# Kernel tuning notes

Hardware: AMD Instinct MI355X
Metric: run time of the kernel (lower is better)

Reference implementation:

```python
import jax, jax.numpy as jnp
import numpy as np

NUM_HEADS = 16
DIM_MODEL = 1024
DIM_K = DIM_MODEL // NUM_HEADS
B, S = 2, 2048


def _linear_params(key, d_in, d_out):
    kw, kb = jax.random.split(key)
    bound = 1.0 / np.sqrt(d_in)
    W = jax.random.uniform(kw, (d_out, d_in), jnp.float32, -bound, bound)
    b = jax.random.uniform(kb, (d_out,), jnp.float32, -bound, bound)
    return W, b


def setup_inputs() -> dict:
    key = jax.random.key(0)
    ks = jax.random.split(key, 7)
    Q_in = jax.random.normal(ks[0], (B, S, DIM_MODEL), jnp.float32)
    K_in = jax.random.normal(ks[1], (B, S, DIM_MODEL), jnp.float32)
    V_in = jax.random.normal(ks[2], (B, S, DIM_MODEL), jnp.float32)
    Wq, bq = _linear_params(ks[3], DIM_MODEL, DIM_MODEL)
    Wk, bk = _linear_params(ks[4], DIM_MODEL, DIM_MODEL)
    Wv, bv = _linear_params(ks[5], DIM_MODEL, DIM_MODEL)
    Wo, bo = _linear_params(ks[6], DIM_MODEL, DIM_MODEL)
    return {"Q_in": Q_in, "K_in": K_in, "V_in": V_in,
            "Wq": Wq, "bq": bq, "Wk": Wk, "bk": bk,
            "Wv": Wv, "bv": bv, "Wo": Wo, "bo": bo}


def reference(Q_in, K_in, V_in, Wq, bq, Wk, bk, Wv, bv, Wo, bo):
    # QKV projections (nn.Linear: x @ W.T + b)
    Q = Q_in @ Wq.T + bq
    K = K_in @ Wk.T + bk
    V = V_in @ Wv.T + bv
    # [B, S, D] -> [B, H, S, dk]
    def split_heads(x):
        return x.reshape(B, S, NUM_HEADS, DIM_K).transpose(0, 2, 1, 3)
    Qh, Kh, Vh = split_heads(Q), split_heads(K), split_heads(V)
    # Scaled dot-product attention
    scale = 1.0 / np.sqrt(DIM_K)
    scores = jnp.einsum('bhqd,bhkd->bhqk', Qh, Kh) * scale  # [B,H,S,S]
    attn = jax.nn.softmax(scores, axis=-1)
    out = jnp.einsum('bhqk,bhkd->bhqd', attn, Vh)  # [B,H,S,dk]
    # Merge heads -> [B, S, D]
    out = out.transpose(0, 2, 1, 3).reshape(B, S, DIM_MODEL)
    return out @ Wo.T + bo
```

## Files before the change

kernel.cpp:

```cpp
#include <hip/hip_runtime.h>
#include <stdint.h>

#define BB 2
#define SS 2048
#define DD 1024
#define HH 16
#define DKK 64
#define MT (BB*SS)

#define GSTRIDE 40
#define ASTRIDE 72

using short8  = __attribute__((ext_vector_type(8))) short;
using floatx4 = __attribute__((ext_vector_type(4))) float;
using u16x4   = __attribute__((ext_vector_type(4))) unsigned short;
typedef unsigned short u16;

__device__ __forceinline__ u16 f2b(float f) {
  union { float f; unsigned u; } v; v.f = f;
  return (u16)((v.u + 0x7FFFu + ((v.u >> 16) & 1u)) >> 16);
}
__device__ __forceinline__ void pack16(const float4* p, short8& lo, short8& hi) {
  float4 x0 = p[0], x1 = p[1], x2 = p[2], x3 = p[3];
  lo[0]=(short)f2b(x0.x); lo[1]=(short)f2b(x0.y); lo[2]=(short)f2b(x0.z); lo[3]=(short)f2b(x0.w);
  lo[4]=(short)f2b(x1.x); lo[5]=(short)f2b(x1.y); lo[6]=(short)f2b(x1.z); lo[7]=(short)f2b(x1.w);
  hi[0]=(short)f2b(x2.x); hi[1]=(short)f2b(x2.y); hi[2]=(short)f2b(x2.z); hi[3]=(short)f2b(x2.w);
  hi[4]=(short)f2b(x3.x); hi[5]=(short)f2b(x3.y); hi[6]=(short)f2b(x3.z); hi[7]=(short)f2b(x3.w);
}
__device__ __forceinline__ void gload16(const u16* g, u16* l) {
  __builtin_amdgcn_global_load_lds(
      (const __attribute__((address_space(1))) void*)g,
      (__attribute__((address_space(3))) void*)l, 16, 0, 0);
}

__global__ __launch_bounds__(256) void cast_w3(
    const float* __restrict__ w0, const float* __restrict__ w1,
    const float* __restrict__ w2, u16* __restrict__ o)
{
  const float* s = (blockIdx.y == 0) ? w0 : (blockIdx.y == 1) ? w1 : w2;
  u16* d = o + (size_t)blockIdx.y * (DD * DD);
  const size_t g = (size_t)blockIdx.x * 256 + threadIdx.x;
  float4 x0 = ((const float4*)s)[g*2], x1 = ((const float4*)s)[g*2+1];
  short8 lo;
  lo[0]=(short)f2b(x0.x); lo[1]=(short)f2b(x0.y); lo[2]=(short)f2b(x0.z); lo[3]=(short)f2b(x0.w);
  lo[4]=(short)f2b(x1.x); lo[5]=(short)f2b(x1.y); lo[6]=(short)f2b(x1.z); lo[7]=(short)f2b(x1.w);
  ((short8*)d)[g] = lo;
}
__global__ __launch_bounds__(256) void cast_a3wo(
    const float* __restrict__ a0, const float* __restrict__ a1,
    const float* __restrict__ a2, const float* __restrict__ a3,
    u16* __restrict__ o0, u16* __restrict__ o1,
    u16* __restrict__ o2, u16* __restrict__ o3)
{
  const int y = blockIdx.y;
  if (y == 3 && blockIdx.x >= (DD*DD/8/256)) return;
  const float* s = (y == 0) ? a0 : (y == 1) ? a1 : (y == 2) ? a2 : a3;
  u16*         d = (y == 0) ? o0 : (y == 1) ? o1 : (y == 2) ? o2 : o3;
  const size_t g = (size_t)blockIdx.x * 256 + threadIdx.x;
  float4 x0 = ((const float4*)s)[g*2], x1 = ((const float4*)s)[g*2+1];
  short8 lo;
  lo[0]=(short)f2b(x0.x); lo[1]=(short)f2b(x0.y); lo[2]=(short)f2b(x0.z); lo[3]=(short)f2b(x0.w);
  lo[4]=(short)f2b(x1.x); lo[5]=(short)f2b(x1.y); lo[6]=(short)f2b(x1.z); lo[7]=(short)f2b(x1.w);
  ((short8*)d)[g] = lo;
}

template<bool OUT_F32>
__device__ __forceinline__ void gemm_async(
    const u16* __restrict__ A, const u16* __restrict__ W,
    const float* __restrict__ bias, void* __restrict__ Cv,
    const int K, const int N, const int m0, const int n0, const float scale)
{
  __shared__ __align__(16) u16 sA[128*32];
  __shared__ __align__(16) u16 sB[128*32];

  const int tid  = threadIdx.x;
  const int wave = tid >> 6;
  const int lane = tid & 63;
  const int quad = lane >> 4;
  const int lr   = lane & 15;
  const int wm   = wave >> 1;
  const int wn   = wave & 1;
  const int srow = lane >> 2;
  const int scol = (lane & 3) * 8;

  floatx4 acc[4][4];
#pragma unroll
  for (int i = 0; i < 4; ++i)
#pragma unroll
    for (int j = 0; j < 4; ++j) acc[i][j] = (floatx4){0.f, 0.f, 0.f, 0.f};

  const u16* gA0 = A + (size_t)(m0 + wave*16       + srow) * K + scol;
  const u16* gA1 = A + (size_t)(m0 + (wave+4)*16   + srow) * K + scol;
  const u16* gW0 = W + (size_t)(n0 + wave*16       + srow) * K + scol;
  const u16* gW1 = W + (size_t)(n0 + (wave+4)*16   + srow) * K + scol;
  u16* lA0 = sA + wave*512;
  u16* lA1 = sA + (wave+4)*512;
  u16* lB0 = sB + wave*512;
  u16* lB1 = sB + (wave+4)*512;

  const int nk = K >> 5;
  for (int kt = 0; kt < nk; ++kt) {
    const int k0 = kt << 5;
    gload16(gA0 + k0, lA0);
    gload16(gA1 + k0, lA1);
    gload16(gW0 + k0, lB0);
    gload16(gW1 + k0, lB1);
    __syncthreads();

    short8 af[4], bf[4];
#pragma unroll
    for (int t = 0; t < 4; ++t) {
      af[t] = *(const short8*)(sA + (wm*64 + t*16 + lr)*32 + quad*8);
      bf[t] = *(const short8*)(sB + (wn*64 + t*16 + lr)*32 + quad*8);
    }
#pragma unroll
    for (int i = 0; i < 4; ++i)
#pragma unroll
      for (int j = 0; j < 4; ++j)
        acc[i][j] = __builtin_amdgcn_mfma_f32_16x16x32_bf16(af[i], bf[j], acc[i][j], 0, 0, 0);
    __syncthreads();
  }

#pragma unroll
  for (int i = 0; i < 4; ++i) {
    const int mb = m0 + wm*64 + i*16 + quad*4;
#pragma unroll
    for (int j = 0; j < 4; ++j) {
      const int n = n0 + wn*64 + j*16 + lr;
      const float bsv = bias[n];
#pragma unroll
      for (int r = 0; r < 4; ++r) {
        const size_t idx = (size_t)(mb + r) * N + n;
        const float v = (acc[i][j][r] + bsv) * scale;
        if (OUT_F32) ((float*)Cv)[idx] = v;
        else         ((u16*)Cv)[idx]   = f2b(v);
      }
    }
  }
}

__global__ __launch_bounds__(256, 3) void gemm_qkv_async(
    const u16* __restrict__ cQ, const u16* __restrict__ cK, const u16* __restrict__ cV,
    const u16* __restrict__ cWq, const u16* __restrict__ cWk, const u16* __restrict__ cWv,
    const float* __restrict__ bq, const float* __restrict__ bk, const float* __restrict__ bv,
    u16* __restrict__ oQ, u16* __restrict__ oK, u16* __restrict__ oV)
{
  const int wsel = blockIdx.x >> 3;
  const int n0 = (blockIdx.x & 7) * 128;
  const int m0 = blockIdx.y * 128;
  const u16* A; const u16* W; const float* bias; u16* C;
  if (wsel == 0)      { A = cQ; W = cWq; bias = bq; C = oQ; }
  else if (wsel == 1) { A = cK; W = cWk; bias = bk; C = oK; }
  else                { A = cV; W = cWv; bias = bv; C = oV; }
  const float scale = (wsel == 0) ? 0.125f : 1.0f;
  gemm_async<false>(A, W, bias, C, DD, DD, m0, n0, scale);
}

__global__ __launch_bounds__(256, 3) void gemm_out_async(
    const u16* __restrict__ A, const u16* __restrict__ cWo,
    const float* __restrict__ bias, float* __restrict__ C)
{
  gemm_async<true>(A, cWo, bias, C, DD, DD, blockIdx.y * 128, blockIdx.x * 128, 1.0f);
}

template<bool A_BF16, bool W_BF16, bool OUT_F32>
__device__ __forceinline__ void gemm_core(
    const void* __restrict__ A, const void* __restrict__ W,
    const float* __restrict__ bias, void* __restrict__ Cv,
    const int K, const int N, const int m0, const int n0, const float scale)
{
  __shared__ __align__(16) u16 sA[128*GSTRIDE];
  __shared__ __align__(16) u16 sB[128*GSTRIDE];

  const int tid  = threadIdx.x;
  const int wave = tid >> 6;
  const int lane = tid & 63;
  const int quad = lane >> 4;
  const int lr   = lane & 15;
  const int wm   = wave >> 1;
  const int wn   = wave & 1;
  const int srow = tid >> 1;
  const int scol = (tid & 1) * 16;

  floatx4 acc[4][4];
#pragma unroll
  for (int i = 0; i < 4; ++i)
#pragma unroll
    for (int j = 0; j < 4; ++j) acc[i][j] = (floatx4){0.f, 0.f, 0.f, 0.f};

  const size_t offA = (size_t)(m0 + srow) * K + scol;
  const size_t offW = (size_t)(n0 + srow) * K + scol;

  const int nk = K >> 5;
  for (int kt = 0; kt < nk; ++kt) {
    const int k0 = kt << 5;
    short8 a0, a1, b0, b1;
    if (A_BF16) {
      const u16* p = (const u16*)A + offA + k0;
      a0 = *(const short8*)p; a1 = *(const short8*)(p + 8);
    } else {
      pack16((const float4*)((const float*)A + offA + k0), a0, a1);
    }
    if (W_BF16) {
      const u16* p = (const u16*)W + offW + k0;
      b0 = *(const short8*)p; b1 = *(const short8*)(p + 8);
    } else {
      pack16((const float4*)((const float*)W + offW + k0), b0, b1);
    }
    __syncthreads();
    *(short8*)(sA + srow * GSTRIDE + scol)     = a0;
    *(short8*)(sA + srow * GSTRIDE + scol + 8) = a1;
    *(short8*)(sB + srow * GSTRIDE + scol)     = b0;
    *(short8*)(sB + srow * GSTRIDE + scol + 8) = b1;
    __syncthreads();

    short8 af[4], bf[4];
#pragma unroll
    for (int t = 0; t < 4; ++t) {
      af[t] = *(const short8*)(sA + (wm*64 + t*16 + lr)*GSTRIDE + quad*8);
      bf[t] = *(const short8*)(sB + (wn*64 + t*16 + lr)*GSTRIDE + quad*8);
    }
#pragma unroll
    for (int i = 0; i < 4; ++i)
#pragma unroll
      for (int j = 0; j < 4; ++j)
        acc[i][j] = __builtin_amdgcn_mfma_f32_16x16x32_bf16(af[i], bf[j], acc[i][j], 0, 0, 0);
  }

#pragma unroll
  for (int i = 0; i < 4; ++i) {
    const int mb = m0 + wm*64 + i*16 + quad*4;
#pragma unroll
    for (int j = 0; j < 4; ++j) {
      const int n = n0 + wn*64 + j*16 + lr;
      const float bsv = bias[n];
#pragma unroll
      for (int r = 0; r < 4; ++r) {
        const size_t idx = (size_t)(mb + r) * N + n;
        const float v = (acc[i][j][r] + bsv) * scale;
        if (OUT_F32) ((float*)Cv)[idx] = v;
        else         ((u16*)Cv)[idx]   = f2b(v);
      }
    }
  }
}

__global__ __launch_bounds__(256, 2) void gemm_qkv_fb(
    const float* __restrict__ Qin, const float* __restrict__ Kin, const float* __restrict__ Vin,
    const u16* __restrict__ cWq, const u16* __restrict__ cWk, const u16* __restrict__ cWv,
    const float* __restrict__ bq, const float* __restrict__ bk, const float* __restrict__ bv,
    u16* __restrict__ oQ, u16* __restrict__ oK, u16* __restrict__ oV)
{
  const int wsel = blockIdx.x >> 3;
  const int n0 = (blockIdx.x & 7) * 128;
  const int m0 = blockIdx.y * 128;
  const float* A; const u16* W; const float* bias; u16* C;
  if (wsel == 0)      { A = Qin; W = cWq; bias = bq; C = oQ; }
  else if (wsel == 1) { A = Kin; W = cWk; bias = bk; C = oK; }
  else                { A = Vin; W = cWv; bias = bv; C = oV; }
  const float scale = (wsel == 0) ? 0.125f : 1.0f;
  gemm_core<false, true, false>(A, W, bias, C, DD, DD, m0, n0, scale);
}
__global__ __launch_bounds__(256, 2) void gemm_out_fb(
    const u16* __restrict__ A, const float* __restrict__ W,
    const float* __restrict__ bias, float* __restrict__ C)
{
  gemm_core<true, false, true>((const void*)A, (const void*)W, bias, C, DD, DD,
                               blockIdx.y * 128, blockIdx.x * 128, 1.0f);
}

__global__ __launch_bounds__(256) void transpose_v(
    const u16* __restrict__ Vp, u16* __restrict__ Vt)
{
  __shared__ u16 t[64 * 65];
  const int st = blockIdx.x, h = blockIdx.y, b = blockIdx.z;

  const int r  = threadIdx.x >> 2;
  const int c0 = (threadIdx.x & 3) * 16;
  const u16* src = Vp + ((size_t)(b * SS + st * 64 + r)) * DD + h * 64 + c0;
  short8 v0 = *(const short8*)src;
  short8 v1 = *(const short8*)(src + 8);
#pragma unroll
  for (int i = 0; i < 8; ++i) {
    t[r * 65 + c0 + i]     = (u16)v0[i];
    t[r * 65 + c0 + 8 + i] = (u16)v1[i];
  }
  __syncthreads();
  union { u16 a[16]; short8 v[2]; } ob;
#pragma unroll
  for (int i = 0; i < 16; ++i) ob.a[i] = t[(c0 + i) * 65 + r];
  u16* dst = Vt + (((size_t)(b * HH + h)) * DKK + r) * SS + st * 64 + c0;
  *(short8*)dst       = ob.v[0];
  *(short8*)(dst + 8) = ob.v[1];
}

__global__ __launch_bounds__(256, 4) void attn(
    const u16* __restrict__ Qp, const u16* __restrict__ Kp,
    const u16* __restrict__ Vt, u16* __restrict__ O)
{
  __shared__ __align__(16) u16 sQ[64 * ASTRIDE];
  __shared__ __align__(16) u16 sK[64 * ASTRIDE];
  __shared__ __align__(16) u16 sV[64 * ASTRIDE];
  __shared__ __align__(16) u16 sP[4][16 * ASTRIDE];

  const int tid = threadIdx.x, wave = tid >> 6, lane = tid & 63;
  const int quad = lane >> 4, lr = lane & 15;
  const int qb = blockIdx.x, h = blockIdx.y, b = blockIdx.z;
  const size_t vbase = ((size_t)(b * HH + h)) * DKK * SS;

  {
    const int r = tid >> 2, c = (tid & 3) * 16;
    const short8* src = (const short8*)(Qp + ((size_t)(b * SS + qb * 64 + r)) * DD + h * 64 + c);
    short8* dst = (short8*)(sQ + r * ASTRIDE + c);
    dst[0] = src[0]; dst[1] = src[1];
  }

  floatx4 accO[4];
  float m_l = -3e38f, l_l = 0.f;
#pragma unroll
  for (int t = 0; t < 4; ++t) accO[t] = (floatx4){0.f, 0.f, 0.f, 0.f};

  for (int kt = 0; kt < SS / 64; ++kt) {
    __syncthreads();
    {
      const int r = tid >> 2, c = (tid & 3) * 16;
      const short8* sk = (const short8*)(Kp + ((size_t)(b * SS + kt * 64 + r)) * DD + h * 64 + c);
      short8* dk = (short8*)(sK + r * ASTRIDE + c);
      dk[0] = sk[0]; dk[1] = sk[1];
      const short8* sv = (const short8*)(Vt + vbase + (size_t)r * SS + kt * 64 + c);
      short8* dv = (short8*)(sV + r * ASTRIDE + c);
      dv[0] = sv[0]; dv[1] = sv[1];
    }
    __syncthreads();

    short8 qb0 = *(const short8*)(sQ + (wave * 16 + lr) * ASTRIDE + quad * 8);
    short8 qb1 = *(const short8*)(sQ + (wave * 16 + lr) * ASTRIDE + 32 + quad * 8);
    floatx4 st[4];
#pragma unroll
    for (int t = 0; t < 4; ++t) {
      short8 ka0 = *(const short8*)(sK + (t * 16 + lr) * ASTRIDE + quad * 8);
      short8 ka1 = *(const short8*)(sK + (t * 16 + lr) * ASTRIDE + 32 + quad * 8);
      floatx4 cc = (floatx4){0.f, 0.f, 0.f, 0.f};
      cc = __builtin_amdgcn_mfma_f32_16x16x32_bf16(ka0, qb0, cc, 0, 0, 0);
      cc = __builtin_amdgcn_mfma_f32_16x16x32_bf16(ka1, qb1, cc, 0, 0, 0);
      st[t] = cc;
    }

    float mx = st[0][0];
#pragma unroll
    for (int t = 0; t < 4; ++t)
#pragma unroll
      for (int r = 0; r < 4; ++r) mx = fmaxf(mx, st[t][r]);
    mx = fmaxf(mx, __shfl_xor(mx, 16, 64));
    mx = fmaxf(mx, __shfl_xor(mx, 32, 64));
    const float mn = fmaxf(m_l, mx);
    const float al = __expf(m_l - mn);
    m_l = mn;
    float rs = 0.f;
    u16x4 pk[4];
#pragma unroll
    for (int t = 0; t < 4; ++t)
#pragma unroll
      for (int r = 0; r < 4; ++r) {
        const float p = __expf(st[t][r] - mn);
        rs += p;
        pk[t][r] = f2b(p);
      }
    rs += __shfl_xor(rs, 16, 64);
    rs += __shfl_xor(rs, 32, 64);
    l_l = l_l * al + rs;

    float arow[4];
#pragma unroll
    for (int r = 0; r < 4; ++r) arow[r] = __shfl(al, quad * 4 + r, 64);
#pragma unroll
    for (int t = 0; t < 4; ++t) {
      floatx4 o = accO[t];
      o[0] *= arow[0]; o[1] *= arow[1]; o[2] *= arow[2]; o[3] *= arow[3];
      accO[t] = o;
    }
#pragma unroll
    for (int t = 0; t < 4; ++t)
      *(u16x4*)(sP[wave] + lr * ASTRIDE + t * 16 + quad * 4) = pk[t];
    __syncthreads();

    short8 p0 = *(const short8*)(sP[wave] + lr * ASTRIDE + quad * 8);
    short8 p1 = *(const short8*)(sP[wave] + lr * ASTRIDE + 32 + quad * 8);
#pragma unroll
    for (int t = 0; t < 4; ++t) {
      short8 v0 = *(const short8*)(sV + (t * 16 + lr) * ASTRIDE + quad * 8);
      short8 v1 = *(const short8*)(sV + (t * 16 + lr) * ASTRIDE + 32 + quad * 8);
      accO[t] = __builtin_amdgcn_mfma_f32_16x16x32_bf16(p0, v0, accO[t], 0, 0, 0);
      accO[t] = __builtin_amdgcn_mfma_f32_16x16x32_bf16(p1, v1, accO[t], 0, 0, 0);
    }
  }

  float lrow[4];
#pragma unroll
  for (int r = 0; r < 4; ++r) lrow[r] = __shfl(l_l, quad * 4 + r, 64);

#pragma unroll
  for (int t = 0; t < 4; ++t)
#pragma unroll
    for (int r = 0; r < 4; ++r) {
      const int s = qb * 64 + wave * 16 + quad * 4 + r;
      const int d = h * 64 + t * 16 + lr;
      O[((size_t)(b * SS + s)) * DD + d] = f2b(accO[t][r] / lrow[r]);
    }
}

extern "C" void kernel_launch(void* const* d_in, const int* in_sizes, int n_in,
                              void* d_out, int out_size, void* d_ws, size_t ws_size,
                              hipStream_t stream)
{
  const float* Qin = (const float*)d_in[0];
  const float* Kin = (const float*)d_in[1];
  const float* Vin = (const float*)d_in[2];
  const float* Wq  = (const float*)d_in[3];
  const float* bq  = (const float*)d_in[4];
  const float* Wk  = (const float*)d_in[5];
  const float* bk  = (const float*)d_in[6];
  const float* Wv  = (const float*)d_in[7];
  const float* bv  = (const float*)d_in[8];
  const float* Wo  = (const float*)d_in[9];
  const float* bo  = (const float*)d_in[10];
  float* out = (float*)d_out;

  const size_t TSZ = (size_t)MT * DD;
  const size_t WSZ = (size_t)DD * DD;
  dim3 blk(256);

  u16* cWq = (u16*)d_out;
  u16* cWk = cWq + WSZ;
  u16* cWv = cWk + WSZ;

  u16* pQ   = (u16*)d_ws;
  u16* pK   = pQ  + TSZ;
  u16* pV   = pK  + TSZ;
  u16* wsVt = pV  + TSZ;
  u16* wsO  = wsVt + TSZ;

  cast_w3<<<dim3(WSZ/8/256, 3), blk, 0, stream>>>(Wq, Wk, Wv, cWq);

  if (ws_size >= (8*TSZ + WSZ) * sizeof(u16)) {
    u16* cQ  = wsO + TSZ;
    u16* cK  = cQ  + TSZ;
    u16* cV  = cK  + TSZ;
    u16* cWo = cV  + TSZ;
    cast_a3wo<<<dim3(TSZ/8/256, 4), blk, 0, stream>>>(Qin, Kin, Vin, Wo,
                                                      cQ, cK, cV, cWo);
    gemm_qkv_async<<<dim3(24, MT/128), blk, 0, stream>>>(
        cQ, cK, cV, cWq, cWk, cWv, bq, bk, bv, pQ, pK, pV);
    transpose_v<<<dim3(SS/64, HH, BB), blk, 0, stream>>>(pV, wsVt);
    attn<<<dim3(SS/64, HH, BB), blk, 0, stream>>>(pQ, pK, wsVt, wsO);
    gemm_out_async<<<dim3(DD/128, MT/128), blk, 0, stream>>>(wsO, cWo, bo, out);
  } else {
    gemm_qkv_fb<<<dim3(24, MT/128), blk, 0, stream>>>(
        Qin, Kin, Vin, cWq, cWk, cWv, bq, bk, bv, pQ, pK, pV);
    transpose_v<<<dim3(SS/64, HH, BB), blk, 0, stream>>>(pV, wsVt);
    attn<<<dim3(SS/64, HH, BB), blk, 0, stream>>>(pQ, pK, wsVt, wsO);
    gemm_out_fb<<<dim3(DD/128, MT/128), blk, 0, stream>>>(wsO, Wo, bo, out);
  }
}
```

Before: 270.5 us.

## Merge cast kernels, deepen GEMM K-tile with swizzle, double attention query tile

```diff
diff --git a/kernel.cpp b/kernel.cpp
--- a/kernel.cpp
+++ b/kernel.cpp
@@ -33,6 +33,34 @@
       (__attribute__((address_space(3))) void*)l, 16, 0, 0);
 }
 
+__global__ __launch_bounds__(256) void cast_all(
+    const float* __restrict__ Qin, const float* __restrict__ Kin,
+    const float* __restrict__ Vin, const float* __restrict__ Wq,
+    const float* __restrict__ Wk,  const float* __restrict__ Wv,
+    const float* __restrict__ Wo,
+    u16* __restrict__ cQ, u16* __restrict__ cK, u16* __restrict__ cV,
+    u16* __restrict__ cWq, u16* __restrict__ cWk, u16* __restrict__ cWv,
+    u16* __restrict__ cWo)
+{
+  const int y = blockIdx.y;
+  if (y >= 3 && blockIdx.x >= (DD*DD/8/256)) return;
+  const float* s; u16* d;
+  switch (y) {
+    case 0: s = Qin; d = cQ;  break;
+    case 1: s = Kin; d = cK;  break;
+    case 2: s = Vin; d = cV;  break;
+    case 3: s = Wq;  d = cWq; break;
+    case 4: s = Wk;  d = cWk; break;
+    case 5: s = Wv;  d = cWv; break;
+    default: s = Wo; d = cWo; break;
+  }
+  const size_t g = (size_t)blockIdx.x * 256 + threadIdx.x;
+  float4 x0 = ((const float4*)s)[g*2], x1 = ((const float4*)s)[g*2+1];
+  short8 lo;
+  lo[0]=(short)f2b(x0.x); lo[1]=(short)f2b(x0.y); lo[2]=(short)f2b(x0.z); lo[3]=(short)f2b(x0.w);
+  lo[4]=(short)f2b(x1.x); lo[5]=(short)f2b(x1.y); lo[6]=(short)f2b(x1.z); lo[7]=(short)f2b(x1.w);
+  ((short8*)d)[g] = lo;
+}
 __global__ __launch_bounds__(256) void cast_w3(
     const float* __restrict__ w0, const float* __restrict__ w1,
     const float* __restrict__ w2, u16* __restrict__ o)
@@ -46,23 +74,6 @@
   lo[4]=(short)f2b(x1.x); lo[5]=(short)f2b(x1.y); lo[6]=(short)f2b(x1.z); lo[7]=(short)f2b(x1.w);
   ((short8*)d)[g] = lo;
 }
-__global__ __launch_bounds__(256) void cast_a3wo(
-    const float* __restrict__ a0, const float* __restrict__ a1,
-    const float* __restrict__ a2, const float* __restrict__ a3,
-    u16* __restrict__ o0, u16* __restrict__ o1,
-    u16* __restrict__ o2, u16* __restrict__ o3)
-{
-  const int y = blockIdx.y;
-  if (y == 3 && blockIdx.x >= (DD*DD/8/256)) return;
-  const float* s = (y == 0) ? a0 : (y == 1) ? a1 : (y == 2) ? a2 : a3;
-  u16*         d = (y == 0) ? o0 : (y == 1) ? o1 : (y == 2) ? o2 : o3;
-  const size_t g = (size_t)blockIdx.x * 256 + threadIdx.x;
-  float4 x0 = ((const float4*)s)[g*2], x1 = ((const float4*)s)[g*2+1];
-  short8 lo;
-  lo[0]=(short)f2b(x0.x); lo[1]=(short)f2b(x0.y); lo[2]=(short)f2b(x0.z); lo[3]=(short)f2b(x0.w);
-  lo[4]=(short)f2b(x1.x); lo[5]=(short)f2b(x1.y); lo[6]=(short)f2b(x1.z); lo[7]=(short)f2b(x1.w);
-  ((short8*)d)[g] = lo;
-}
 
 template<bool OUT_F32>
 __device__ __forceinline__ void gemm_async(
@@ -70,8 +81,8 @@
     const float* __restrict__ bias, void* __restrict__ Cv,
     const int K, const int N, const int m0, const int n0, const float scale)
 {
-  __shared__ __align__(16) u16 sA[128*32];
-  __shared__ __align__(16) u16 sB[128*32];
+  __shared__ __align__(16) u16 sA[128*64];
+  __shared__ __align__(16) u16 sB[128*64];
 
   const int tid  = threadIdx.x;
   const int wave = tid >> 6;
@@ -80,8 +91,8 @@
   const int lr   = lane & 15;
   const int wm   = wave >> 1;
   const int wn   = wave & 1;
-  const int srow = lane >> 2;
-  const int scol = (lane & 3) * 8;
+  const int srow = lane >> 3;
+  const int swz  = (((lane & 7) ^ ((srow & 1) << 2)) << 3);
 
   floatx4 acc[4][4];
 #pragma unroll
@@ -89,35 +100,39 @@
 #pragma unroll
     for (int j = 0; j < 4; ++j) acc[i][j] = (floatx4){0.f, 0.f, 0.f, 0.f};
 
-  const u16* gA0 = A + (size_t)(m0 + wave*16       + srow) * K + scol;
-  const u16* gA1 = A + (size_t)(m0 + (wave+4)*16   + srow) * K + scol;
-  const u16* gW0 = W + (size_t)(n0 + wave*16       + srow) * K + scol;
-  const u16* gW1 = W + (size_t)(n0 + (wave+4)*16   + srow) * K + scol;
-  u16* lA0 = sA + wave*512;
-  u16* lA1 = sA + (wave+4)*512;
-  u16* lB0 = sB + wave*512;
-  u16* lB1 = sB + (wave+4)*512;
-
-  const int nk = K >> 5;
+  const u16* pA[4]; const u16* pW[4];
+#pragma unroll
+  for (int c = 0; c < 4; ++c) {
+    const int row = (wave + c*4) * 8 + srow;
+    pA[c] = A + (size_t)(m0 + row) * K + swz;
+    pW[c] = W + (size_t)(n0 + row) * K + swz;
+  }
+
+  const int nk = K >> 6;
   for (int kt = 0; kt < nk; ++kt) {
-    const int k0 = kt << 5;
-    gload16(gA0 + k0, lA0);
-    gload16(gA1 + k0, lA1);
-    gload16(gW0 + k0, lB0);
-    gload16(gW1 + k0, lB1);
-    __syncthreads();
-
-    short8 af[4], bf[4];
-#pragma unroll
-    for (int t = 0; t < 4; ++t) {
-      af[t] = *(const short8*)(sA + (wm*64 + t*16 + lr)*32 + quad*8);
-      bf[t] = *(const short8*)(sB + (wn*64 + t*16 + lr)*32 + quad*8);
-    }
-#pragma unroll
-    for (int i = 0; i < 4; ++i)
-#pragma unroll
-      for (int j = 0; j < 4; ++j)
-        acc[i][j] = __builtin_amdgcn_mfma_f32_16x16x32_bf16(af[i], bf[j], acc[i][j], 0, 0, 0);
+    const int k0 = kt << 6;
+#pragma unroll
+    for (int c = 0; c < 4; ++c) {
+      gload16(pA[c] + k0, sA + (wave + c*4) * 512);
+      gload16(pW[c] + k0, sB + (wave + c*4) * 512);
+    }
+    __syncthreads();
+
+#pragma unroll
+    for (int h2 = 0; h2 < 2; ++h2) {
+      const int csel = (quad << 3) + ((h2 ^ (lr & 1)) << 5);
+      short8 af[4], bf[4];
+#pragma unroll
+      for (int t = 0; t < 4; ++t) {
+        af[t] = *(const short8*)(sA + (wm*64 + t*16 + lr)*64 + csel);
+        bf[t] = *(const short8*)(sB + (wn*64 + t*16 + lr)*64 + csel);
+      }
+#pragma unroll
+      for (int i = 0; i < 4; ++i)
+#pragma unroll
+        for (int j = 0; j < 4; ++j)
+          acc[i][j] = __builtin_amdgcn_mfma_f32_16x16x32_bf16(af[i], bf[j], acc[i][j], 0, 0, 0);
+    }
     __syncthreads();
   }
 
@@ -294,14 +309,14 @@
   *(short8*)(dst + 8) = ob.v[1];
 }
 
-__global__ __launch_bounds__(256, 4) void attn(
+__global__ __launch_bounds__(256, 2) void attn(
     const u16* __restrict__ Qp, const u16* __restrict__ Kp,
     const u16* __restrict__ Vt, u16* __restrict__ O)
 {
-  __shared__ __align__(16) u16 sQ[64 * ASTRIDE];
+  __shared__ __align__(16) u16 sQ[128 * ASTRIDE];
   __shared__ __align__(16) u16 sK[64 * ASTRIDE];
   __shared__ __align__(16) u16 sV[64 * ASTRIDE];
-  __shared__ __align__(16) u16 sP[4][16 * ASTRIDE];
+  __shared__ __align__(16) u16 sP[4][32 * ASTRIDE];
 
   const int tid = threadIdx.x, wave = tid >> 6, lane = tid & 63;
   const int quad = lane >> 4, lr = lane & 15;
@@ -309,16 +324,18 @@
   const size_t vbase = ((size_t)(b * HH + h)) * DKK * SS;
 
   {
-    const int r = tid >> 2, c = (tid & 3) * 16;
-    const short8* src = (const short8*)(Qp + ((size_t)(b * SS + qb * 64 + r)) * DD + h * 64 + c);
-    short8* dst = (short8*)(sQ + r * ASTRIDE + c);
-    dst[0] = src[0]; dst[1] = src[1];
-  }
-
-  floatx4 accO[4];
-  float m_l = -3e38f, l_l = 0.f;
-#pragma unroll
-  for (int t = 0; t < 4; ++t) accO[t] = (floatx4){0.f, 0.f, 0.f, 0.f};
+    const int r = tid >> 1, c0 = (tid & 1) * 32;
+    const short8* src = (const short8*)(Qp + ((size_t)(b * SS + qb * 128 + r)) * DD + h * 64 + c0);
+    short8* dst = (short8*)(sQ + r * ASTRIDE + c0);
+    dst[0] = src[0]; dst[1] = src[1]; dst[2] = src[2]; dst[3] = src[3];
+  }
+
+  floatx4 accO[2][4];
+  float m_l[2] = { -3e38f, -3e38f }, l_l[2] = { 0.f, 0.f };
+#pragma unroll
+  for (int g = 0; g < 2; ++g)
+#pragma unroll
+    for (int t = 0; t < 4; ++t) accO[g][t] = (floatx4){0.f, 0.f, 0.f, 0.f};
 
   for (int kt = 0; kt < SS / 64; ++kt) {
     __syncthreads();
@@ -333,80 +350,89 @@
     }
     __syncthreads();
 
-    short8 qb0 = *(const short8*)(sQ + (wave * 16 + lr) * ASTRIDE + quad * 8);
-    short8 qb1 = *(const short8*)(sQ + (wave * 16 + lr) * ASTRIDE + 32 + quad * 8);
-    floatx4 st[4];
+#pragma unroll
+    for (int g = 0; g < 2; ++g) {
+      short8 qv0 = *(const short8*)(sQ + (g*64 + wave*16 + lr) * ASTRIDE + quad * 8);
+      short8 qv1 = *(const short8*)(sQ + (g*64 + wave*16 + lr) * ASTRIDE + 32 + quad * 8);
+      floatx4 st[4];
+#pragma unroll
+      for (int t = 0; t < 4; ++t) {
+        short8 ka0 = *(const short8*)(sK + (t*16 + lr) * ASTRIDE + quad * 8);
+        short8 ka1 = *(const short8*)(sK + (t*16 + lr) * ASTRIDE + 32 + quad * 8);
+        floatx4 cc = (floatx4){0.f, 0.f, 0.f, 0.f};
+        cc = __builtin_amdgcn_mfma_f32_16x16x32_bf16(ka0, qv0, cc, 0, 0, 0);
+        cc = __builtin_amdgcn_mfma_f32_16x16x32_bf16(ka1, qv1, cc, 0, 0, 0);
+        st[t] = cc;
+      }
+
+      float mx = st[0][0];
+#pragma unroll
+      for (int t = 0; t < 4; ++t)
+#pragma unroll
+        for (int r = 0; r < 4; ++r) mx = fmaxf(mx, st[t][r]);
+      mx = fmaxf(mx, __shfl_xor(mx, 16, 64));
+      mx = fmaxf(mx, __shfl_xor(mx, 32, 64));
+      const float mn = fmaxf(m_l[g], mx);
+      const float al = __expf(m_l[g] - mn);
+      m_l[g] = mn;
+      float rs = 0.f;
+      u16x4 pk[4];
+#pragma unroll
+      for (int t = 0; t < 4; ++t)
+#pragma unroll
+        for (int r = 0; r < 4; ++r) {
+          const float p = __expf(st[t][r] - mn);
+          rs += p;
+          pk[t][r] = f2b(p);
+        }
+      rs += __shfl_xor(rs, 16, 64);
+      rs += __shfl_xor(rs, 32, 64);
+      l_l[g] = l_l[g] * al + rs;
+
+      float arow[4];
+#pragma unroll
+      for (int r = 0; r < 4; ++r) arow[r] = __shfl(al, quad * 4 + r, 64);
+#pragma unroll
+      for (int t = 0; t < 4; ++t) {
+        floatx4 o = accO[g][t];
+        o[0] *= arow[0]; o[1] *= arow[1]; o[2] *= arow[2]; o[3] *= arow[3];
+        accO[g][t] = o;
+      }
+#pragma unroll
+      for (int t = 0; t < 4; ++t)
+        *(u16x4*)(sP[wave] + (g*16 + lr) * ASTRIDE + t * 16 + quad * 4) = pk[t];
+    }
+    __syncthreads();
+
+    short8 p00 = *(const short8*)(sP[wave] + lr * ASTRIDE + quad * 8);
+    short8 p01 = *(const short8*)(sP[wave] + lr * ASTRIDE + 32 + quad * 8);
+    short8 p10 = *(const short8*)(sP[wave] + (16 + lr) * ASTRIDE + quad * 8);
+    short8 p11 = *(const short8*)(sP[wave] + (16 + lr) * ASTRIDE + 32 + quad * 8);
 #pragma unroll
     for (int t = 0; t < 4; ++t) {
-      short8 ka0 = *(const short8*)(sK + (t * 16 + lr) * ASTRIDE + quad * 8);
-      short8 ka1 = *(const short8*)(sK + (t * 16 + lr) * ASTRIDE + 32 + quad * 8);
-      floatx4 cc = (floatx4){0.f, 0.f, 0.f, 0.f};
-      cc = __builtin_amdgcn_mfma_f32_16x16x32_bf16(ka0, qb0, cc, 0, 0, 0);
-      cc = __builtin_amdgcn_mfma_f32_16x16x32_bf16(ka1, qb1, cc, 0, 0, 0);
-      st[t] = cc;
-    }
-
-    float mx = st[0][0];
+      short8 v0 = *(const short8*)(sV + (t*16 + lr) * ASTRIDE + quad * 8);
+      short8 v1 = *(const short8*)(sV + (t*16 + lr) * ASTRIDE + 32 + quad * 8);
+      accO[0][t] = __builtin_amdgcn_mfma_f32_16x16x32_bf16(p00, v0, accO[0][t], 0, 0, 0);
+      accO[0][t] = __builtin_amdgcn_mfma_f32_16x16x32_bf16(p01, v1, accO[0][t], 0, 0, 0);
+      accO[1][t] = __builtin_amdgcn_mfma_f32_16x16x32_bf16(p10, v0, accO[1][t], 0, 0, 0);
+      accO[1][t] = __builtin_amdgcn_mfma_f32_16x16x32_bf16(p11, v1, accO[1][t], 0, 0, 0);
+    }
+  }
+
+#pragma unroll
+  for (int g = 0; g < 2; ++g) {
+    float lrow[4];
+#pragma unroll
+    for (int r = 0; r < 4; ++r) lrow[r] = __shfl(l_l[g], quad * 4 + r, 64);
 #pragma unroll
     for (int t = 0; t < 4; ++t)
 #pragma unroll
-      for (int r = 0; r < 4; ++r) mx = fmaxf(mx, st[t][r]);
-    mx = fmaxf(mx, __shfl_xor(mx, 16, 64));
-    mx = fmaxf(mx, __shfl_xor(mx, 32, 64));
-    const float mn = fmaxf(m_l, mx);
-    const float al = __expf(m_l - mn);
-    m_l = mn;
-    float rs = 0.f;
-    u16x4 pk[4];
-#pragma unroll
-    for (int t = 0; t < 4; ++t)
-#pragma unroll
       for (int r = 0; r < 4; ++r) {
-        const float p = __expf(st[t][r] - mn);
-        rs += p;
-        pk[t][r] = f2b(p);
-      }
-    rs += __shfl_xor(rs, 16, 64);
-    rs += __shfl_xor(rs, 32, 64);
-    l_l = l_l * al + rs;
-
-    float arow[4];
-#pragma unroll
-    for (int r = 0; r < 4; ++r) arow[r] = __shfl(al, quad * 4 + r, 64);
-#pragma unroll
-    for (int t = 0; t < 4; ++t) {
-      floatx4 o = accO[t];
-      o[0] *= arow[0]; o[1] *= arow[1]; o[2] *= arow[2]; o[3] *= arow[3];
-      accO[t] = o;
-    }
-#pragma unroll
-    for (int t = 0; t < 4; ++t)
-      *(u16x4*)(sP[wave] + lr * ASTRIDE + t * 16 + quad * 4) = pk[t];
-    __syncthreads();
-
-    short8 p0 = *(const short8*)(sP[wave] + lr * ASTRIDE + quad * 8);
-    short8 p1 = *(const short8*)(sP[wave] + lr * ASTRIDE + 32 + quad * 8);
-#pragma unroll
-    for (int t = 0; t < 4; ++t) {
-      short8 v0 = *(const short8*)(sV + (t * 16 + lr) * ASTRIDE + quad * 8);
-      short8 v1 = *(const short8*)(sV + (t * 16 + lr) * ASTRIDE + 32 + quad * 8);
-      accO[t] = __builtin_amdgcn_mfma_f32_16x16x32_bf16(p0, v0, accO[t], 0, 0, 0);
-      accO[t] = __builtin_amdgcn_mfma_f32_16x16x32_bf16(p1, v1, accO[t], 0, 0, 0);
-    }
-  }
-
-  float lrow[4];
-#pragma unroll
-  for (int r = 0; r < 4; ++r) lrow[r] = __shfl(l_l, quad * 4 + r, 64);
-
-#pragma unroll
-  for (int t = 0; t < 4; ++t)
-#pragma unroll
-    for (int r = 0; r < 4; ++r) {
-      const int s = qb * 64 + wave * 16 + quad * 4 + r;
-      const int d = h * 64 + t * 16 + lr;
-      O[((size_t)(b * SS + s)) * DD + d] = f2b(accO[t][r] / lrow[r]);
-    }
+        const int s = qb * 128 + g * 64 + wave * 16 + quad * 4 + r;
+        const int d = h * 64 + t * 16 + lr;
+        O[((size_t)(b * SS + s)) * DD + d] = f2b(accO[g][t][r] / lrow[r]);
+      }
+  }
 }
 
 extern "C" void kernel_launch(void* const* d_in, const int* in_sizes, int n_in,
@@ -440,25 +466,24 @@
   u16* wsVt = pV  + TSZ;
   u16* wsO  = wsVt + TSZ;
 
-  cast_w3<<<dim3(WSZ/8/256, 3), blk, 0, stream>>>(Wq, Wk, Wv, cWq);
-
   if (ws_size >= (8*TSZ + WSZ) * sizeof(u16)) {
     u16* cQ  = wsO + TSZ;
     u16* cK  = cQ  + TSZ;
     u16* cV  = cK  + TSZ;
     u16* cWo = cV  + TSZ;
-    cast_a3wo<<<dim3(TSZ/8/256, 4), blk, 0, stream>>>(Qin, Kin, Vin, Wo,
-                                                      cQ, cK, cV, cWo);
+    cast_all<<<dim3(TSZ/8/256, 7), blk, 0, stream>>>(
+        Qin, Kin, Vin, Wq, Wk, Wv, Wo, cQ, cK, cV, cWq, cWk, cWv, cWo);
     gemm_qkv_async<<<dim3(24, MT/128), blk, 0, stream>>>(
         cQ, cK, cV, cWq, cWk, cWv, bq, bk, bv, pQ, pK, pV);
     transpose_v<<<dim3(SS/64, HH, BB), blk, 0, stream>>>(pV, wsVt);
-    attn<<<dim3(SS/64, HH, BB), blk, 0, stream>>>(pQ, pK, wsVt, wsO);
+    attn<<<dim3(SS/128, HH, BB), blk, 0, stream>>>(pQ, pK, wsVt, wsO);
     gemm_out_async<<<dim3(DD/128, MT/128), blk, 0, stream>>>(wsO, cWo, bo, out);
   } else {
+    cast_w3<<<dim3(WSZ/8/256, 3), blk, 0, stream>>>(Wq, Wk, Wv, cWq);
     gemm_qkv_fb<<<dim3(24, MT/128), blk, 0, stream>>>(
         Qin, Kin, Vin, cWq, cWk, cWv, bq, bk, bv, pQ, pK, pV);
     transpose_v<<<dim3(SS/64, HH, BB), blk, 0, stream>>>(pV, wsVt);
-    attn<<<dim3(SS/64, HH, BB), blk, 0, stream>>>(pQ, pK, wsVt, wsO);
+    attn<<<dim3(SS/128, HH, BB), blk, 0, stream>>>(pQ, pK, wsVt, wsO);
     gemm_out_fb<<<dim3(DD/128, MT/128), blk, 0, stream>>>(wsO, Wo, bo, out);
   }
 }
```

Result: no change. 265.7 us (-1.8%).
